# Performance work log

Measured on AMD Instinct MI355X. Metric: run time of the kernel, lower is better.

Reference implementation:

```python
import jax, jax.numpy as jnp
import numpy as np

H = 16          # num_heads
EPS = 1e-5      # LayerNorm eps (torch default)


def _layernorm(x, g, b):
    m = jnp.mean(x, axis=-1, keepdims=True)
    v = jnp.mean((x - m) ** 2, axis=-1, keepdims=True)
    return (x - m) * jax.lax.rsqrt(v + EPS) * g + b


def setup_inputs() -> dict:
    key = jax.random.key(0)
    ks = jax.random.split(key, 16)
    B, S, D, F = 4, 1024, 1024, 4096
    s = 0.02
    inp = {
        "x": jax.random.normal(ks[0], (B, S, D), jnp.float32),
        "attn_bias": jax.random.normal(ks[1], (B - 1, H), jnp.float32),
        "mask": jax.random.randint(ks[2], (B, 1, S, S), 0, 2).astype(jnp.float32),
        "ln1_g": jnp.ones((D,), jnp.float32),
        "ln1_b": jnp.zeros((D,), jnp.float32),
        "Wq": jax.random.normal(ks[3], (D, D), jnp.float32) * s,
        "bq": jnp.zeros((D,), jnp.float32),
        "Wk": jax.random.normal(ks[4], (D, D), jnp.float32) * s,
        "bk": jnp.zeros((D,), jnp.float32),
        "Wv": jax.random.normal(ks[5], (D, D), jnp.float32) * s,
        "bv": jnp.zeros((D,), jnp.float32),
        "Wo": jax.random.normal(ks[6], (D, D), jnp.float32) * s,
        "bo": jnp.zeros((D,), jnp.float32),
        "ln2_g": jnp.ones((D,), jnp.float32),
        "ln2_b": jnp.zeros((D,), jnp.float32),
        "W1": jax.random.normal(ks[7], (D, F), jnp.float32) * s,
        "b1": jnp.zeros((F,), jnp.float32),
        "W2": jax.random.normal(ks[8], (F, D), jnp.float32) * s,
        "b2": jnp.zeros((D,), jnp.float32),
    }
    return inp


def reference(x, attn_bias, mask, ln1_g, ln1_b, Wq, bq, Wk, bk, Wv, bv, Wo, bo,
              ln2_g, ln2_b, W1, b1, W2, b2):
    B, S, D = x.shape
    d = D // H
    scale = d ** -0.5

    # ---- self-attention block ----
    y = _layernorm(x, ln1_g, ln1_b)
    q = (y @ Wq + bq).reshape(B, S, H, d).transpose(0, 2, 1, 3) * scale  # [B,H,S,d]
    k = (y @ Wk + bk).reshape(B, S, H, d).transpose(0, 2, 1, 3)
    v = (y @ Wv + bv).reshape(B, S, H, d).transpose(0, 2, 1, 3)

    scores = jnp.einsum("bhqd,bhkd->bhqk", q, k)                         # [B,H,S,S]
    # per-batch additive bias applied to batches 1: only (as in torch x[1:] += bias)
    scores = scores.at[1:].add(attn_bias[:, :, None, None])
    # multiplicative mask + large-negative additive mask where mask <= 0
    scores = scores * mask + jnp.where(mask > 0.0, 0.0, -1e9)
    attn = jax.nn.softmax(scores, axis=-1)

    ctx = jnp.einsum("bhqk,bhkd->bhqd", attn, v)                          # [B,H,S,d]
    ctx = ctx.transpose(0, 2, 1, 3).reshape(B, S, D)
    x = x + (ctx @ Wo + bo)

    # ---- FFN block ----
    y = _layernorm(x, ln2_g, ln2_b)
    y = jax.nn.gelu(y @ W1 + b1, approximate=False) @ W2 + b2
    return x + y
```

## Files before the change

### kernel.cpp

```cpp
#include <hip/hip_runtime.h>
#include <hip/hip_bf16.h>
#include <math.h>

typedef __attribute__((ext_vector_type(8))) __bf16 bf16x8;
typedef __attribute__((ext_vector_type(4))) float f32x4;
typedef __hip_bfloat16 bf16;

#define D_MODEL 1024
#define F_FFN   4096
#define NHEAD   16
#define HDIM    64
#define SEQ     1024
#define BATCH   4

static __device__ __forceinline__ unsigned short bf_bits(bf16 h) {
  return __builtin_bit_cast(unsigned short, h);
}

template <int N>
static __device__ __forceinline__ void vwait() {
  asm volatile("s_waitcnt vmcnt(%0)" :: "n"(N) : "memory");
}

static __device__ __forceinline__ void gload_lds16(const bf16* src, bf16* dst) {
  __builtin_amdgcn_global_load_lds(
      (const __attribute__((address_space(1))) void*)src,
      (__attribute__((address_space(3))) void*)dst, 16, 0, 0);
}

static __device__ __forceinline__ float gelu_fast(float x) {
  float u = x * (0.7978845608f + 0.0356774081f * x * x);
  u = fminf(u, 15.f);
  float e = __expf(2.f * u);
  return 0.5f * x * (1.f + (e - 1.f) / (e + 1.f));
}

__global__ __launch_bounds__(1024) void prep_kernel(
    const float* __restrict__ Wq, const float* __restrict__ Wk,
    const float* __restrict__ Wv, const float* __restrict__ Wo,
    const float* __restrict__ W1, const float* __restrict__ W2,
    const float* __restrict__ mask,
    bf16* __restrict__ Wqkv_t, bf16* __restrict__ Wo_t,
    bf16* __restrict__ W1_t, bf16* __restrict__ W2_t,
    unsigned* __restrict__ mbits) {
  __shared__ float tile[32][33];
  int bid = blockIdx.x;
  int tid = threadIdx.x;
  if (bid < 12288) {
    const float* W; bf16* Wt; int K, N, tx32, ty32;
    if (bid < 4096) {
      int w = bid >> 10;
      W  = (w == 0) ? Wq : (w == 1) ? Wk : (w == 2) ? Wv : Wo;
      Wt = (w < 3) ? Wqkv_t + (size_t)w * 1024 * 1024 : Wo_t;
      K = 1024; N = 1024;
      int t = bid & 1023; tx32 = t & 31; ty32 = t >> 5;
    } else if (bid < 8192) {
      W = W1; Wt = W1_t; K = 1024; N = 4096;
      int t = bid - 4096; tx32 = t & 127; ty32 = t >> 7;
    } else {
      W = W2; Wt = W2_t; K = 4096; N = 1024;
      int t = bid - 8192; tx32 = t & 31; ty32 = t >> 5;
    }
    int nb = tx32 * 32, kb = ty32 * 32;
    int tx = tid & 31, ty = tid >> 5;
    tile[ty][tx] = W[(size_t)(kb + ty) * N + nb + tx];
    __syncthreads();
    Wt[(size_t)(nb + ty) * K + kb + tx] = __float2bfloat16(tile[tx][ty]);
  } else {
    int gw = ((bid - 12288) * 1024 + tid) >> 6;
    int lane = tid & 63;
    const float4 m = reinterpret_cast<const float4*>(mask)[(size_t)gw * 64 + lane];
    unsigned long long b0 = __ballot(m.x > 0.f);
    unsigned long long b1 = __ballot(m.y > 0.f);
    unsigned long long b2 = __ballot(m.z > 0.f);
    unsigned long long b3 = __ballot(m.w > 0.f);
    if (lane < 8) {
      unsigned v = 0;
#pragma unroll
      for (int i = 0; i < 8; ++i) {
        int srcl = lane * 8 + i;
        v |= (((unsigned)(b0 >> srcl) & 1u) << (i * 4 + 0));
        v |= (((unsigned)(b1 >> srcl) & 1u) << (i * 4 + 1));
        v |= (((unsigned)(b2 >> srcl) & 1u) << (i * 4 + 2));
        v |= (((unsigned)(b3 >> srcl) & 1u) << (i * 4 + 3));
      }
      mbits[(size_t)gw * 8 + lane] = v;
    }
  }
}

__global__ __launch_bounds__(256) void layernorm_kernel(
    const float* __restrict__ x, const float* __restrict__ g,
    const float* __restrict__ bt, bf16* __restrict__ y) {
  int row = blockIdx.x;
  int tid = threadIdx.x;
  const float* xr = x + (size_t)row * D_MODEL;
  float4 v = reinterpret_cast<const float4*>(xr)[tid];
  float s  = v.x + v.y + v.z + v.w;
  float s2 = v.x * v.x + v.y * v.y + v.z * v.z + v.w * v.w;
  for (int o = 32; o; o >>= 1) { s += __shfl_xor(s, o); s2 += __shfl_xor(s2, o); }
  __shared__ float r1[4], r2[4];
  int wid = tid >> 6, lane = tid & 63;
  if (lane == 0) { r1[wid] = s; r2[wid] = s2; }
  __syncthreads();
  float tot  = r1[0] + r1[1] + r1[2] + r1[3];
  float tot2 = r2[0] + r2[1] + r2[2] + r2[3];
  float mean = tot * (1.f / D_MODEL);
  float var  = tot2 * (1.f / D_MODEL) - mean * mean;
  float rstd = rsqrtf(var + 1e-5f);
  float4 gg = reinterpret_cast<const float4*>(g)[tid];
  float4 bb = reinterpret_cast<const float4*>(bt)[tid];
  ushort4 o;
  o.x = bf_bits(__float2bfloat16((v.x - mean) * rstd * gg.x + bb.x));
  o.y = bf_bits(__float2bfloat16((v.y - mean) * rstd * gg.y + bb.y));
  o.z = bf_bits(__float2bfloat16((v.z - mean) * rstd * gg.z + bb.z));
  o.w = bf_bits(__float2bfloat16((v.w - mean) * rstd * gg.w + bb.w));
  reinterpret_cast<ushort4*>(y + (size_t)row * D_MODEL)[tid] = o;
}

enum { MODE_QKV = 0, MODE_O = 1, MODE_GELU = 2, MODE_OUT = 3 };

__global__ __launch_bounds__(1024, 1) void gemm256sq_gelu_kernel(
    const bf16* __restrict__ A, const bf16* __restrict__ Bt,
    int M, int N, int K,
    const float* __restrict__ bias0, bf16* __restrict__ out_bf) {
  constexpr int R = 3;
  __shared__ bf16 AS[R][256 * 32];
  __shared__ bf16 BS[R][256 * 32];
  int tid = threadIdx.x;
  int wid = tid >> 6, lane = tid & 63;
  int wm4 = wid >> 2, wn4 = wid & 3;
  int lrow = lane & 15, lg = lane >> 4;
  int nwg = gridDim.x * gridDim.y;
  int lin = blockIdx.y * gridDim.x + blockIdx.x;
  int swz = (lin & 7) * (nwg >> 3) + (lin >> 3);
  int bxi = swz % gridDim.x, byi = swz / gridDim.x;
  int bm = byi * 256, bn = bxi * 256;
  int srow = tid >> 2;
  int sg = (tid & 3) ^ ((tid >> 3) & 3);
  const bf16* Asrc = A  + (size_t)bm * K + sg * 8;
  const bf16* Bsrc = Bt + (size_t)bn * K + sg * 8;
  f32x4 acc[4][4] = {};
  const int NT = K / 32;

  auto stage = [&](int t, int slot) {
    int k0 = t * 32;
    gload_lds16(Asrc + (size_t)srow * K + k0, &AS[slot][tid * 8]);
    gload_lds16(Bsrc + (size_t)srow * K + k0, &BS[slot][tid * 8]);
  };

  int sw = (lg ^ ((lrow >> 1) & 3)) << 4;
  stage(0, 0);
  stage(1, 1);
  int rslot = 0, wslot = 2;
  for (int t = 0; t < NT; ++t) {
    if (t < NT - 1) vwait<2>();
    else            vwait<0>();
    __builtin_amdgcn_s_barrier();
    const char* as = (const char*)AS[rslot];
    const char* bs = (const char*)BS[rslot];
    bf16x8 af[4], bfr[4];
#pragma unroll
    for (int f = 0; f < 4; ++f)
      af[f] = *reinterpret_cast<const bf16x8*>(as + (wm4 * 64 + f * 16 + lrow) * 64 + sw);
#pragma unroll
    for (int g = 0; g < 4; ++g)
      bfr[g] = *reinterpret_cast<const bf16x8*>(bs + (wn4 * 64 + g * 16 + lrow) * 64 + sw);
    if (t + 2 < NT) stage(t + 2, wslot);
    __builtin_amdgcn_s_setprio(1);
#pragma unroll
    for (int f = 0; f < 4; ++f)
#pragma unroll
      for (int g = 0; g < 4; ++g)
        acc[f][g] = __builtin_amdgcn_mfma_f32_16x16x32_bf16(af[f], bfr[g], acc[f][g], 0, 0, 0);
    __builtin_amdgcn_s_setprio(0);
    rslot = (rslot == R - 1) ? 0 : rslot + 1;
    wslot = (wslot == R - 1) ? 0 : wslot + 1;
  }

#pragma unroll
  for (int f = 0; f < 4; ++f) {
#pragma unroll
    for (int g = 0; g < 4; ++g) {
#pragma unroll
      for (int r = 0; r < 4; ++r) {
        int row = bm + wm4 * 64 + f * 16 + lg * 4 + r;
        int col = bn + wn4 * 64 + g * 16 + lrow;
        float tv = acc[f][g][r] + bias0[col];
        out_bf[(size_t)row * N + col] = __float2bfloat16(gelu_fast(tv));
      }
    }
  }
}

template <int MODE, int TN>
__global__ __launch_bounds__(512, 4) void gemm256_kernel(
    const bf16* __restrict__ A, const bf16* __restrict__ Bt,
    int M, int N, int K,
    const float* __restrict__ bias0, const float* __restrict__ bias1,
    const float* __restrict__ bias2,
    const float* __restrict__ resid,
    bf16* __restrict__ out_q, bf16* __restrict__ out_k, bf16* __restrict__ out_vt,
    float* __restrict__ out_f) {
  constexpr int R = 3;
  constexpr int NF = TN / 32;
  __shared__ bf16 AS[R][256 * 32];
  __shared__ bf16 BS[R][TN * 32];
  int tid = threadIdx.x;
  int wid = tid >> 6, lane = tid & 63;
  int wm4 = wid >> 1, wn2 = wid & 1;
  int lrow = lane & 15, lg = lane >> 4;
  int nwg = gridDim.x * gridDim.y;
  int lin = blockIdx.y * gridDim.x + blockIdx.x;
  int swz = (lin & 7) * (nwg >> 3) + (lin >> 3);
  int bxi = swz % gridDim.x, byi = swz / gridDim.x;
  int bm = byi * 256, bn = bxi * TN;
  int srow = tid >> 2;
  int sg = (tid & 3) ^ ((tid >> 3) & 3);
  const bf16* Asrc = A  + (size_t)bm * K + sg * 8;
  const bf16* Bsrc = Bt + (size_t)bn * K + sg * 8;
  f32x4 acc[4][NF] = {};
  const int NT = K / 32;

  auto stage = [&](int t, int slot) {
    int k0 = t * 32;
#pragma unroll
    for (int j = 0; j < 2; ++j) {
      int row = j * 128 + srow;
      gload_lds16(Asrc + (size_t)row * K + k0, &AS[slot][(j * 512 + tid) * 8]);
    }
    if (TN == 128) {
      gload_lds16(Bsrc + (size_t)srow * K + k0, &BS[slot][tid * 8]);
    } else {
      if (wid < 4)
        gload_lds16(Bsrc + (size_t)srow * K + k0, &BS[slot][tid * 8]);
    }
  };

  int sw = (lg ^ ((lrow >> 1) & 3)) << 4;
  stage(0, 0);
  stage(1, 1);
  int rslot = 0, wslot = 2;
  for (int t = 0; t < NT; ++t) {
    if (t < NT - 1) {
      if (TN == 128) { vwait<3>(); }
      else { if (wid < 4) vwait<3>(); else vwait<2>(); }
    } else {
      vwait<0>();
    }
    __builtin_amdgcn_s_barrier();
    const char* as = (const char*)AS[rslot];
    const char* bs = (const char*)BS[rslot];
    bf16x8 af[4], bfr[NF];
#pragma unroll
    for (int f = 0; f < 4; ++f)
      af[f] = *reinterpret_cast<const bf16x8*>(as + (wm4 * 64 + f * 16 + lrow) * 64 + sw);
#pragma unroll
    for (int g = 0; g < NF; ++g)
      bfr[g] = *reinterpret_cast<const bf16x8*>(bs + (wn2 * (TN / 2) + g * 16 + lrow) * 64 + sw);
    if (t + 2 < NT) stage(t + 2, wslot);
    __builtin_amdgcn_s_setprio(1);
#pragma unroll
    for (int f = 0; f < 4; ++f)
#pragma unroll
      for (int g = 0; g < NF; ++g)
        acc[f][g] = __builtin_amdgcn_mfma_f32_16x16x32_bf16(af[f], bfr[g], acc[f][g], 0, 0, 0);
    __builtin_amdgcn_s_setprio(0);
    rslot = (rslot == R - 1) ? 0 : rslot + 1;
    wslot = (wslot == R - 1) ? 0 : wslot + 1;
  }

#pragma unroll
  for (int f = 0; f < 4; ++f) {
#pragma unroll
    for (int g = 0; g < NF; ++g) {
#pragma unroll
      for (int r = 0; r < 4; ++r) {
        int row = bm + wm4 * 64 + f * 16 + lg * 4 + r;
        int col = bn + wn2 * (TN / 2) + g * 16 + lrow;
        float v = acc[f][g][r];
        if (MODE == MODE_QKV) {
          if (col < 1024) {
            out_q[(size_t)row * 1024 + col] = __float2bfloat16((v + bias0[col]) * 0.125f);
          } else if (col < 2048) {
            out_k[(size_t)row * 1024 + (col - 1024)] = __float2bfloat16(v + bias1[col - 1024]);
          } else {
            int d = col - 2048;
            int b = row >> 10;
            int s = row & 1023;
            out_vt[((size_t)(b << 10) + d) * 1024 + s] = __float2bfloat16(v + bias2[d]);
          }
        } else {
          out_f[(size_t)row * N + col] = resid[(size_t)row * N + col] + v + bias0[col];
        }
      }
    }
  }
}

#define KVB 64
__global__ __launch_bounds__(512) void attn_kernel(
    const bf16* __restrict__ q, const bf16* __restrict__ k,
    const bf16* __restrict__ vt, const unsigned* __restrict__ mbits,
    bf16* __restrict__ ctx) {
  __shared__ bf16 Kt[2][KVB * 64];
  __shared__ bf16 Vt[2][KVB * 64];
  __shared__ bf16 P[8][16 * 64];
  int tid = threadIdx.x, wid = tid >> 6, lane = tid & 63;
  int blk = (blockIdx.x & 7) * 64 + (blockIdx.x >> 3);
  int qblk = blk & 7, h = (blk >> 3) & 15, b = blk >> 7;
  int qs = qblk * 128 + wid * 16;
  int lrow = lane & 15, lg = lane >> 4;

  size_t qoff = ((size_t)(b * SEQ + qs + lrow)) * D_MODEL + h * HDIM;
  bf16x8 qa0 = *reinterpret_cast<const bf16x8*>(q + qoff + lg * 8);
  bf16x8 qa1 = *reinterpret_cast<const bf16x8*>(q + qoff + 32 + lg * 8);

  float ps[4] = {0.f, 0.f, 0.f, 0.f};
  f32x4 O[4] = {};
  const unsigned* mb = mbits + ((size_t)(b * SEQ + qs + lg * 4)) * 32;
  bf16* Pw = P[wid];

  int rr = lane >> 3;
  int sg8 = (lane & 7) ^ rr;
  const bf16* kb_src = k + ((size_t)b * SEQ) * D_MODEL + h * HDIM + sg8 * 8;
  const bf16* vb_src = vt + ((size_t)(b * D_MODEL + h * HDIM)) * SEQ + sg8 * 8;

#define STAGE(KT2, BUF)                                                          \
  {                                                                              \
    int ks2 = (KT2) * KVB;                                                       \
    gload_lds16(kb_src + (size_t)(ks2 + wid * 8 + rr) * D_MODEL,                 \
                &Kt[BUF][wid * 512]);                                            \
    gload_lds16(vb_src + (size_t)(wid * 8 + rr) * SEQ + ks2,                     \
                &Vt[BUF][wid * 512]);                                            \
  }

  STAGE(0, 0);
  for (int kt = 0; kt < SEQ / KVB; ++kt) {
    int cur = kt & 1;
    __syncthreads();
    if (kt < SEQ / KVB - 1) STAGE(kt + 1, cur ^ 1);

    f32x4 sc[4];
#pragma unroll
    for (int c = 0; c < 4; ++c) {
      int krow = c * 16 + lrow;
      const char* kp = (const char*)&Kt[cur][krow * 64];
      bf16x8 kb0 = *reinterpret_cast<const bf16x8*>(kp + ((lg ^ (krow & 7)) << 4));
      bf16x8 kb1 = *reinterpret_cast<const bf16x8*>(kp + ((((lg + 4) & 7) ^ (krow & 7)) << 4));
      f32x4 z = {0.f, 0.f, 0.f, 0.f};
      sc[c] = __builtin_amdgcn_mfma_f32_16x16x32_bf16(qa0, kb0, z, 0, 0, 0);
      sc[c] = __builtin_amdgcn_mfma_f32_16x16x32_bf16(qa1, kb1, sc[c], 0, 0, 0);
    }

#pragma unroll
    for (int r = 0; r < 4; ++r) {
      uint2 w = *reinterpret_cast<const uint2*>(mb + (size_t)r * 32 + kt * 2);
      int prow = lg * 4 + r;
      char* pb = (char*)Pw + prow * 128;
#pragma unroll
      for (int c = 0; c < 4; ++c) {
        unsigned wsel = (c >= 2) ? w.y : w.x;
        unsigned keep = (wsel >> ((c & 1) * 16 + lrow)) & 1u;
        float p = keep ? __expf(sc[c][r]) : 0.f;
        ps[r] += p;
        int pcol = c * 16 + lrow;
        *(__bf16*)(pb + (((pcol >> 3) ^ (prow & 7)) << 4) + (pcol & 7) * 2) =
            __float2bfloat16(p);
      }
    }

    const char* pbase = (const char*)Pw + lrow * 128;
    bf16x8 pa0 = *reinterpret_cast<const bf16x8*>(pbase + ((lg ^ (lrow & 7)) << 4));
    bf16x8 pa1 = *reinterpret_cast<const bf16x8*>(pbase + ((((lg + 4) & 7) ^ (lrow & 7)) << 4));
#pragma unroll
    for (int nb = 0; nb < 4; ++nb) {
      int vrow = nb * 16 + lrow;
      const char* vp = (const char*)&Vt[cur][vrow * 64];
      bf16x8 vb0 = *reinterpret_cast<const bf16x8*>(vp + ((lg ^ (vrow & 7)) << 4));
      bf16x8 vb1 = *reinterpret_cast<const bf16x8*>(vp + ((((lg + 4) & 7) ^ (vrow & 7)) << 4));
      O[nb] = __builtin_amdgcn_mfma_f32_16x16x32_bf16(pa0, vb0, O[nb], 0, 0, 0);
      O[nb] = __builtin_amdgcn_mfma_f32_16x16x32_bf16(pa1, vb1, O[nb], 0, 0, 0);
    }
  }
#undef STAGE

#pragma unroll
  for (int o = 1; o < 16; o <<= 1)
#pragma unroll
    for (int r = 0; r < 4; ++r) ps[r] += __shfl_xor(ps[r], o);
#pragma unroll
  for (int nb = 0; nb < 4; ++nb)
#pragma unroll
    for (int r = 0; r < 4; ++r) {
      int qg = qs + lg * 4 + r;
      ctx[((size_t)(b * SEQ + qg)) * D_MODEL + h * HDIM + nb * 16 + lrow] =
          __float2bfloat16(O[nb][r] / ps[r]);
    }
}

extern "C" void kernel_launch(void* const* d_in, const int* in_sizes, int n_in,
                              void* d_out, int out_size, void* d_ws, size_t ws_size,
                              hipStream_t stream) {
  const float* x        = (const float*)d_in[0];
  const float* mask     = (const float*)d_in[2];
  const float* ln1_g    = (const float*)d_in[3];
  const float* ln1_b    = (const float*)d_in[4];
  const float* Wq       = (const float*)d_in[5];
  const float* bq       = (const float*)d_in[6];
  const float* Wk       = (const float*)d_in[7];
  const float* bk       = (const float*)d_in[8];
  const float* Wv       = (const float*)d_in[9];
  const float* bv       = (const float*)d_in[10];
  const float* Wo       = (const float*)d_in[11];
  const float* bo       = (const float*)d_in[12];
  const float* ln2_g    = (const float*)d_in[13];
  const float* ln2_b    = (const float*)d_in[14];
  const float* W1       = (const float*)d_in[15];
  const float* b1       = (const float*)d_in[16];
  const float* W2       = (const float*)d_in[17];
  const float* b2       = (const float*)d_in[18];
  float* out            = (float*)d_out;

  char* w = (char*)d_ws;
  const size_t MB = 1u << 20;
  bf16*     y      = (bf16*)(w + 0);
  bf16*     qb     = (bf16*)(w + 8 * MB);
  bf16*     kb     = (bf16*)(w + 16 * MB);
  bf16*     vt     = (bf16*)(w + 24 * MB);
  bf16*     hbuf   = (bf16*)(w + 0);
  bf16*     Wqkv_t = (bf16*)(w + 32 * MB);
  bf16*     Wo_t   = (bf16*)(w + 38 * MB);
  bf16*     W1_t   = (bf16*)(w + 40 * MB);
  bf16*     W2_t   = (bf16*)(w + 48 * MB);
  bf16*     ctx    = (bf16*)(w + 56 * MB);
  float*    x2     = (float*)(w + 64 * MB);
  unsigned* mbits  = (unsigned*)(w + 64 * MB);
  bf16*     y2     = (bf16*)(w + 80 * MB);
  (void)in_sizes; (void)n_in; (void)out_size; (void)ws_size;

  prep_kernel<<<13312, 1024, 0, stream>>>(Wq, Wk, Wv, Wo, W1, W2, mask,
                                          Wqkv_t, Wo_t, W1_t, W2_t, mbits);

  layernorm_kernel<<<4096, 256, 0, stream>>>(x, ln1_g, ln1_b, y);

  gemm256_kernel<MODE_QKV, 128><<<dim3(24, 16), 512, 0, stream>>>(
      y, Wqkv_t, 4096, 3072, 1024, bq, bk, bv, nullptr,
      qb, kb, vt, nullptr);

  attn_kernel<<<512, 512, 0, stream>>>(qb, kb, vt, mbits, ctx);

  gemm256_kernel<MODE_O, 64><<<dim3(16, 16), 512, 0, stream>>>(
      ctx, Wo_t, 4096, 1024, 1024, bo, nullptr, nullptr, x,
      nullptr, nullptr, nullptr, x2);

  layernorm_kernel<<<4096, 256, 0, stream>>>(x2, ln2_g, ln2_b, y2);

  gemm256sq_gelu_kernel<<<dim3(16, 16), 1024, 0, stream>>>(
      y2, W1_t, 4096, 4096, 1024, b1, hbuf);

  gemm256_kernel<MODE_OUT, 64><<<dim3(16, 16), 512, 0, stream>>>(
      hbuf, W2_t, 4096, 1024, 4096, b2, nullptr, nullptr, x2,
      nullptr, nullptr, nullptr, out);
}
```

Before: 245.3 us.

## Split-K the FFN down-projection and deepen the FFN-up GEMM LDS pipeline

The final W2 GEMM (K=4096) is split into two K-halves. This doubles the workgroup count to 512 and gives better CU fill. Each half writes bf16 partial sums, and a new elementwise kernel adds the partials, bias and residual. The W1 GELU GEMM also moves from a 3-slot to a 4-slot LDS ring with prefetch distance 3. Rounding partial sums to bf16 costs some accuracy, and the extra reduce pass adds memory traffic and a launch.

```diff
diff --git a/kernel.cpp b/kernel.cpp
--- a/kernel.cpp
+++ b/kernel.cpp
@@ -15,6 +15,10 @@
 
 static __device__ __forceinline__ unsigned short bf_bits(bf16 h) {
   return __builtin_bit_cast(unsigned short, h);
+}
+static __device__ __forceinline__ float bf2f(unsigned short u) {
+  unsigned v = (unsigned)u << 16;
+  return __builtin_bit_cast(float, v);
 }
 
 template <int N>
@@ -118,13 +122,13 @@
   reinterpret_cast<ushort4*>(y + (size_t)row * D_MODEL)[tid] = o;
 }
 
-enum { MODE_QKV = 0, MODE_O = 1, MODE_GELU = 2, MODE_OUT = 3 };
+enum { MODE_QKV = 0, MODE_O = 1 };
 
 __global__ __launch_bounds__(1024, 1) void gemm256sq_gelu_kernel(
     const bf16* __restrict__ A, const bf16* __restrict__ Bt,
     int M, int N, int K,
     const float* __restrict__ bias0, bf16* __restrict__ out_bf) {
-  constexpr int R = 3;
+  constexpr int R = 4;
   __shared__ bf16 AS[R][256 * 32];
   __shared__ bf16 BS[R][256 * 32];
   int tid = threadIdx.x;
@@ -143,22 +147,23 @@
   f32x4 acc[4][4] = {};
   const int NT = K / 32;
 
-  auto stage = [&](int t, int slot) {
+  auto stage = [&](int t) {
+    int slot = t & 3;
     int k0 = t * 32;
     gload_lds16(Asrc + (size_t)srow * K + k0, &AS[slot][tid * 8]);
     gload_lds16(Bsrc + (size_t)srow * K + k0, &BS[slot][tid * 8]);
   };
 
   int sw = (lg ^ ((lrow >> 1) & 3)) << 4;
-  stage(0, 0);
-  stage(1, 1);
-  int rslot = 0, wslot = 2;
+  stage(0); stage(1); stage(2);
   for (int t = 0; t < NT; ++t) {
-    if (t < NT - 1) vwait<2>();
-    else            vwait<0>();
+    if (t < NT - 2)       vwait<4>();
+    else if (t == NT - 2) vwait<2>();
+    else                  vwait<0>();
     __builtin_amdgcn_s_barrier();
-    const char* as = (const char*)AS[rslot];
-    const char* bs = (const char*)BS[rslot];
+    int slot = t & 3;
+    const char* as = (const char*)AS[slot];
+    const char* bs = (const char*)BS[slot];
     bf16x8 af[4], bfr[4];
 #pragma unroll
     for (int f = 0; f < 4; ++f)
@@ -166,7 +171,7 @@
 #pragma unroll
     for (int g = 0; g < 4; ++g)
       bfr[g] = *reinterpret_cast<const bf16x8*>(bs + (wn4 * 64 + g * 16 + lrow) * 64 + sw);
-    if (t + 2 < NT) stage(t + 2, wslot);
+    if (t + 3 < NT) stage(t + 3);
     __builtin_amdgcn_s_setprio(1);
 #pragma unroll
     for (int f = 0; f < 4; ++f)
@@ -174,8 +179,6 @@
       for (int g = 0; g < 4; ++g)
         acc[f][g] = __builtin_amdgcn_mfma_f32_16x16x32_bf16(af[f], bfr[g], acc[f][g], 0, 0, 0);
     __builtin_amdgcn_s_setprio(0);
-    rslot = (rslot == R - 1) ? 0 : rslot + 1;
-    wslot = (wslot == R - 1) ? 0 : wslot + 1;
   }
 
 #pragma unroll
@@ -191,6 +194,106 @@
       }
     }
   }
+}
+
+__global__ __launch_bounds__(512, 2) void gemm_out_split_kernel(
+    const bf16* __restrict__ A, const bf16* __restrict__ Bt, int K,
+    bf16* __restrict__ psum0, bf16* __restrict__ psum1) {
+  constexpr int R = 4;
+  __shared__ bf16 AS[R][256 * 32];
+  __shared__ bf16 BS[R][64 * 32];
+  int tid = threadIdx.x;
+  int wid = tid >> 6, lane = tid & 63;
+  int wm4 = wid >> 1, wn2 = wid & 1;
+  int lrow = lane & 15, lg = lane >> 4;
+  int nwg = gridDim.x * gridDim.y;
+  int lin = blockIdx.y * gridDim.x + blockIdx.x;
+  int swz = (lin & 7) * (nwg >> 3) + (lin >> 3);
+  int bxi = swz & 15;
+  int rest = swz >> 4;
+  int byi = rest & 15, z = rest >> 4;
+  int bm = byi * 256, bn = bxi * 64;
+  int kbeg = z * 2048;
+  bf16* psum = z ? psum1 : psum0;
+  int srow = tid >> 2;
+  int sg = (tid & 3) ^ ((tid >> 3) & 3);
+  const bf16* Asrc = A  + (size_t)bm * K + kbeg + sg * 8;
+  const bf16* Bsrc = Bt + (size_t)bn * K + kbeg + sg * 8;
+  f32x4 acc[4][2] = {};
+  const int NT = 2048 / 32;
+
+  auto stage = [&](int t) {
+    int slot = t & 3;
+    int k0 = t * 32;
+#pragma unroll
+    for (int j = 0; j < 2; ++j) {
+      int row = j * 128 + srow;
+      gload_lds16(Asrc + (size_t)row * K + k0, &AS[slot][(j * 512 + tid) * 8]);
+    }
+    if (wid < 4)
+      gload_lds16(Bsrc + (size_t)srow * K + k0, &BS[slot][tid * 8]);
+  };
+
+  int sw = (lg ^ ((lrow >> 1) & 3)) << 4;
+  stage(0); stage(1); stage(2);
+  for (int t = 0; t < NT; ++t) {
+    if (t < NT - 2) {
+      if (wid < 4) vwait<6>(); else vwait<4>();
+    } else if (t == NT - 2) {
+      if (wid < 4) vwait<3>(); else vwait<2>();
+    } else {
+      vwait<0>();
+    }
+    __builtin_amdgcn_s_barrier();
+    int slot = t & 3;
+    const char* as = (const char*)AS[slot];
+    const char* bs = (const char*)BS[slot];
+    bf16x8 af[4], bfr[2];
+#pragma unroll
+    for (int f = 0; f < 4; ++f)
+      af[f] = *reinterpret_cast<const bf16x8*>(as + (wm4 * 64 + f * 16 + lrow) * 64 + sw);
+#pragma unroll
+    for (int g = 0; g < 2; ++g)
+      bfr[g] = *reinterpret_cast<const bf16x8*>(bs + (wn2 * 32 + g * 16 + lrow) * 64 + sw);
+    if (t + 3 < NT) stage(t + 3);
+    __builtin_amdgcn_s_setprio(1);
+#pragma unroll
+    for (int f = 0; f < 4; ++f)
+#pragma unroll
+      for (int g = 0; g < 2; ++g)
+        acc[f][g] = __builtin_amdgcn_mfma_f32_16x16x32_bf16(af[f], bfr[g], acc[f][g], 0, 0, 0);
+    __builtin_amdgcn_s_setprio(0);
+  }
+
+#pragma unroll
+  for (int f = 0; f < 4; ++f) {
+#pragma unroll
+    for (int g = 0; g < 2; ++g) {
+#pragma unroll
+      for (int r = 0; r < 4; ++r) {
+        int row = bm + wm4 * 64 + f * 16 + lg * 4 + r;
+        int col = bn + wn2 * 32 + g * 16 + lrow;
+        psum[(size_t)row * 1024 + col] = __float2bfloat16(acc[f][g][r]);
+      }
+    }
+  }
+}
+
+__global__ __launch_bounds__(256) void reduce_out_kernel(
+    const float* __restrict__ x2, const float* __restrict__ b2,
+    const bf16* __restrict__ p0, const bf16* __restrict__ p1,
+    float* __restrict__ out) {
+  int i = blockIdx.x * 256 + threadIdx.x;
+  float4 xv = reinterpret_cast<const float4*>(x2)[i];
+  ushort4 a = reinterpret_cast<const ushort4*>(p0)[i];
+  ushort4 b = reinterpret_cast<const ushort4*>(p1)[i];
+  float4 bias = reinterpret_cast<const float4*>(b2)[i & 255];
+  float4 o;
+  o.x = xv.x + bias.x + bf2f(a.x) + bf2f(b.x);
+  o.y = xv.y + bias.y + bf2f(a.y) + bf2f(b.y);
+  o.z = xv.z + bias.z + bf2f(a.z) + bf2f(b.z);
+  o.w = xv.w + bias.w + bf2f(a.w) + bf2f(b.w);
+  reinterpret_cast<float4*>(out)[i] = o;
 }
 
 template <int MODE, int TN>
@@ -437,6 +540,8 @@
   float*    x2     = (float*)(w + 64 * MB);
   unsigned* mbits  = (unsigned*)(w + 64 * MB);
   bf16*     y2     = (bf16*)(w + 80 * MB);
+  bf16*     psum0  = (bf16*)(w + 56 * MB);
+  bf16*     psum1  = (bf16*)(w + 80 * MB);
   (void)in_sizes; (void)n_in; (void)out_size; (void)ws_size;
 
   prep_kernel<<<13312, 1024, 0, stream>>>(Wq, Wk, Wv, Wo, W1, W2, mask,
@@ -459,7 +564,8 @@
   gemm256sq_gelu_kernel<<<dim3(16, 16), 1024, 0, stream>>>(
       y2, W1_t, 4096, 4096, 1024, b1, hbuf);
 
-  gemm256_kernel<MODE_OUT, 64><<<dim3(16, 16), 512, 0, stream>>>(
-      hbuf, W2_t, 4096, 1024, 4096, b2, nullptr, nullptr, x2,
-      nullptr, nullptr, nullptr, out);
-}
+  gemm_out_split_kernel<<<dim3(16, 32), 512, 0, stream>>>(
+      hbuf, W2_t, 4096, psum0, psum1);
+
+  reduce_out_kernel<<<4096, 256, 0, stream>>>(x2, b2, psum0, psum1, out);
+}
```

After: 240.0 us. -2.1%, faster.
